# Optimization experiments

Hardware: AMD Instinct MI355X
Metric: run time of the kernel (lower is better)

The kernel has to match this reference:

```python
import jax, jax.numpy as jnp
import numpy as np

N = 6720      # 16 graphs * 420 nodes
E = 33600     # 16 graphs * 2100 edges (5 per node)
DIN = 2048
H1, C1 = 2, 1024   # conv1: heads=2, out=1024 -> concat 2048
H2, C2 = 1, 64     # conv2: heads=1, out=64
ED = 64            # edge_dim
NODES_PER_GRAPH = 420


def _lin(k, fi, fo):
    return jax.random.normal(k, (fi, fo), jnp.float32) / np.sqrt(fi).astype(np.float32)


def setup_inputs() -> dict:
    key = jax.random.key(0)
    ks = jax.random.split(key, 24)
    d = {}
    d["x"] = jax.random.normal(ks[0], (N, DIN), jnp.float32)
    d["edge_index"] = jax.random.randint(ks[1], (2, E), 0, N)
    # tiled learned edge_features param (torch.rand init), one 2100xED block per graph
    ef = jax.random.uniform(ks[2], (5 * NODES_PER_GRAPH, ED), jnp.float32)
    d["edge_attr"] = jnp.tile(ef, (N // NODES_PER_GRAPH, 1))
    HC1 = H1 * C1
    d["q1_w"] = _lin(ks[3], DIN, HC1); d["q1_b"] = jax.random.normal(ks[4], (HC1,)) * 0.01
    d["k1_w"] = _lin(ks[5], DIN, HC1); d["k1_b"] = jax.random.normal(ks[6], (HC1,)) * 0.01
    d["v1_w"] = _lin(ks[7], DIN, HC1); d["v1_b"] = jax.random.normal(ks[8], (HC1,)) * 0.01
    d["e1_w"] = _lin(ks[9], ED, HC1)                      # lin_edge has no bias in PyG
    d["s1_w"] = _lin(ks[10], DIN, HC1); d["s1_b"] = jax.random.normal(ks[11], (HC1,)) * 0.01
    HC2 = H2 * C2
    d["q2_w"] = _lin(ks[12], HC1, HC2); d["q2_b"] = jax.random.normal(ks[13], (HC2,)) * 0.01
    d["k2_w"] = _lin(ks[14], HC1, HC2); d["k2_b"] = jax.random.normal(ks[15], (HC2,)) * 0.01
    d["v2_w"] = _lin(ks[16], HC1, HC2); d["v2_b"] = jax.random.normal(ks[17], (HC2,)) * 0.01
    d["e2_w"] = _lin(ks[18], ED, HC2)
    d["s2_w"] = _lin(ks[19], HC1, HC2); d["s2_b"] = jax.random.normal(ks[20], (HC2,)) * 0.01
    return d


def _transformer_conv(x, src, dst, edge_attr, qw, qb, kw, kb, vw, vb, ew, sw, sb, H, C):
    """PyG TransformerConv (concat=True, beta=False, root_weight=True)."""
    n = x.shape[0]
    q = (x @ qw + qb).reshape(n, H, C)
    k = (x @ kw + kb).reshape(n, H, C)
    v = (x @ vw + vb).reshape(n, H, C)
    e = (edge_attr @ ew).reshape(-1, H, C)         # [E,H,C]
    kj = k[src] + e                                # gather source keys + edge emb
    alpha = jnp.sum(q[dst] * kj, axis=-1) / np.sqrt(C).astype(np.float32)  # [E,H]
    # scatter-softmax over incoming edges of each target node
    amax = jax.ops.segment_max(alpha, dst, num_segments=n)   # [N,H]
    ex = jnp.exp(alpha - amax[dst])
    denom = jax.ops.segment_sum(ex, dst, num_segments=n)
    attn = ex / (denom[dst] + 1e-16)               # [E,H]
    msg = (v[src] + e) * attn[..., None]           # [E,H,C]
    out = jax.ops.segment_sum(msg, dst, num_segments=n).reshape(n, H * C)
    return out + x @ sw + sb                       # root/skip connection


def reference(x, edge_index, edge_attr,
              q1_w, q1_b, k1_w, k1_b, v1_w, v1_b, e1_w, s1_w, s1_b,
              q2_w, q2_b, k2_w, k2_b, v2_w, v2_b, e2_w, s2_w, s2_b):
    src, dst = edge_index[0], edge_index[1]
    h = jax.nn.relu(_transformer_conv(x, src, dst, edge_attr,
                                      q1_w, q1_b, k1_w, k1_b, v1_w, v1_b,
                                      e1_w, s1_w, s1_b, H1, C1))
    h = jax.nn.relu(_transformer_conv(h, src, dst, edge_attr,
                                      q2_w, q2_b, k2_w, k2_b, v2_w, v2_b,
                                      e2_w, s2_w, s2_b, H2, C2))
    return h.reshape(-1, NODES_PER_GRAPH * 64)     # forward returns here (fc layers are dead code)
```

## Files before the change

kernel.cpp:

```cpp
#include <hip/hip_runtime.h>
#include <hip/hip_bf16.h>
#include <cstdint>
#include <cstddef>

#define NN    6720
#define MPAD  6912
#define NE    33600
#define KDIM  2048
#define HC1   2048

typedef __attribute__((ext_vector_type(8))) short bhalf8;
typedef __attribute__((ext_vector_type(4))) float fx4;

__device__ __forceinline__ float bf2f(short s) {
    union { unsigned int u; float f; } c;
    c.u = ((unsigned int)(unsigned short)s) << 16;
    return c.f;
}

__device__ __forceinline__ void gload16(const __hip_bfloat16* g, void* lds)
{
    __builtin_amdgcn_global_load_lds(
        (const __attribute__((address_space(1))) unsigned int*)g,
        (__attribute__((address_space(3))) unsigned int*)lds,
        16, 0, 0);
}

#define CFENCE asm volatile("" ::: "memory")

__global__ __launch_bounds__(256, 3) void gemm128_fused(
    const __hip_bfloat16* __restrict__ A,
    const __hip_bfloat16* __restrict__ Bt,
    const float* __restrict__ bcat,
    __hip_bfloat16* __restrict__ oq,
    __hip_bfloat16* __restrict__ ok,
    __hip_bfloat16* __restrict__ ov,
    float* __restrict__ oh)
{
    __shared__ alignas(16) char Lds[49152];

    const int bid = blockIdx.x;
    const int i   = bid >> 3;
    const int bx  = (bid & 7) * 8 + (i & 7);
    const int by  = i >> 3;

    const int tid  = threadIdx.x;
    const int w    = tid >> 6;
    const int lane = tid & 63;
    const int wm = w >> 1, wn = w & 1;
    const int rowA = by * 128;
    const int rowB = bx * 128;

    const int sug = ((lane & 3) ^ ((lane >> 3) & 3)) << 3;
    const __hip_bfloat16* Ag0 = A  + (size_t)(rowA + w * 32 + (lane >> 2)) * KDIM + sug;
    const __hip_bfloat16* Bg0 = Bt + (size_t)(rowB + w * 32 + (lane >> 2)) * KDIM + sug;

    const int rds = (((lane >> 4) ^ (((lane & 15) >> 1) & 3)) << 4);

    fx4 acc[4][4] = {};

#define STAGE(T)                                                          \
    { const int s_ = (T) % 3; const int k0_ = (T) * 32;                   \
      char* ab_ = Lds + s_ * 8192 + w * 2048;                             \
      char* bb_ = Lds + 24576 + s_ * 8192 + w * 2048;                     \
      gload16(Ag0 + k0_, ab_);                                            \
      gload16(Ag0 + k0_ + 16 * KDIM, ab_ + 1024);                         \
      gload16(Bg0 + k0_, bb_);                                            \
      gload16(Bg0 + k0_ + 16 * KDIM, bb_ + 1024); }

#define TILE(T, VM, DOSTAGE)                                              \
    { if (DOSTAGE) { STAGE((T) + 2); }                                    \
      asm volatile("s_waitcnt vmcnt(" VM ")" ::: "memory");               \
      __builtin_amdgcn_s_barrier(); CFENCE;                               \
      const int s_ = (T) % 3;                                             \
      const char* ap_ = Lds + s_ * 8192;                                  \
      const char* bp_ = Lds + 24576 + s_ * 8192;                          \
      bhalf8 af_[4], bf_[4];                                              \
      _Pragma("unroll")                                                   \
      for (int nj = 0; nj < 4; ++nj)                                      \
          bf_[nj] = *(const bhalf8*)(bp_ + (wn * 64 + nj * 16 + (lane & 15)) * 64 + rds); \
      _Pragma("unroll")                                                   \
      for (int mi = 0; mi < 4; ++mi)                                      \
          af_[mi] = *(const bhalf8*)(ap_ + (wm * 64 + mi * 16 + (lane & 15)) * 64 + rds); \
      __builtin_amdgcn_s_setprio(1);                                      \
      _Pragma("unroll")                                                   \
      for (int mi = 0; mi < 4; ++mi)                                      \
          _Pragma("unroll")                                               \
          for (int nj = 0; nj < 4; ++nj)                                  \
              acc[mi][nj] = __builtin_amdgcn_mfma_f32_16x16x32_bf16(      \
                  af_[mi], bf_[nj], acc[mi][nj], 0, 0, 0);                \
      __builtin_amdgcn_s_setprio(0); CFENCE;                              \
      __builtin_amdgcn_s_barrier(); CFENCE; }

    STAGE(0); STAGE(1);
    for (int t = 0; t < (KDIM / 32) - 2; ++t) {
        TILE(t, "8", 1);
    }
    TILE((KDIM / 32) - 2, "4", 0);
    TILE((KDIM / 32) - 1, "0", 0);

#undef TILE
#undef STAGE

    const int gcol = rowB + wn * 64;
    const int seg  = gcol >> 11;
    const int lcol = gcol & 2047;
    float bv[4];
    #pragma unroll
    for (int nj = 0; nj < 4; ++nj) bv[nj] = bcat[gcol + nj * 16 + (lane & 15)];
    char* scr = Lds + w * 8192;
    const int growA = rowA + wm * 64;

    #pragma unroll
    for (int h = 0; h < 2; ++h) {
        #pragma unroll
        for (int m2 = 0; m2 < 2; ++m2) {
            const int mi = h * 2 + m2;
            #pragma unroll
            for (int nj = 0; nj < 4; ++nj) {
                const int cl = nj * 16 + (lane & 15);
                #pragma unroll
                for (int i2 = 0; i2 < 4; ++i2) {
                    const int rl = m2 * 16 + ((lane >> 4) << 2) + i2;
                    *(float*)(scr + rl * 256 + cl * 4) = acc[mi][nj][i2] + bv[nj];
                }
            }
        }
        CFENCE;
        if (seg < 3) {
            __hip_bfloat16* dst = (seg == 0) ? oq : (seg == 1) ? ok : ov;
            #pragma unroll
            for (int p = 0; p < 4; ++p) {
                const int rl = p * 8 + (lane >> 3);
                const int u  = lane & 7;
                const float4 f0 = *(const float4*)(scr + rl * 256 + u * 32);
                const float4 f1 = *(const float4*)(scr + rl * 256 + u * 32 + 16);
                __hip_bfloat16 tb[8];
                tb[0] = __float2bfloat16(f0.x); tb[1] = __float2bfloat16(f0.y);
                tb[2] = __float2bfloat16(f0.z); tb[3] = __float2bfloat16(f0.w);
                tb[4] = __float2bfloat16(f1.x); tb[5] = __float2bfloat16(f1.y);
                tb[6] = __float2bfloat16(f1.z); tb[7] = __float2bfloat16(f1.w);
                *(bhalf8*)&dst[(size_t)(growA + h * 32 + rl) * 2048 + lcol + u * 8] =
                    *(bhalf8*)tb;
            }
        } else {
            #pragma unroll
            for (int p = 0; p < 8; ++p) {
                const int rl = p * 4 + (lane >> 4);
                const int u  = lane & 15;
                const float4 f = *(const float4*)(scr + rl * 256 + u * 16);
                *(float4*)&oh[(size_t)(growA + h * 32 + rl) * 2048 + lcol + u * 4] = f;
            }
        }
        asm volatile("s_waitcnt lgkmcnt(0)" ::: "memory");
        CFENCE;
    }
}

__global__ __launch_bounds__(256) void gemm_bf16(
    const __hip_bfloat16* __restrict__ A,
    const __hip_bfloat16* __restrict__ Bt,
    const float* __restrict__ bias,
    float* __restrict__ C,
    __hip_bfloat16* __restrict__ Cb,
    int M, int N, int K, int flags)
{
    __shared__ alignas(16) __hip_bfloat16 Asm[128 * 64];
    __shared__ alignas(16) __hip_bfloat16 Bsm[128 * 64];
    const int tid  = threadIdx.x;
    const int w    = tid >> 6;
    const int lane = tid & 63;
    const int wr = w >> 1, wc = w & 1;
    const int rowA = blockIdx.y * 128;
    const int rowB = blockIdx.x * 128;
    const int klen = K / gridDim.z;
    const int kbeg = blockIdx.z * klen;

    const int srow = w * 32 + (lane >> 3);
    const int ug8  = ((lane & 7) ^ (lane >> 3)) << 3;
    const __hip_bfloat16* Ag = A  + (size_t)(rowA + srow) * K + ug8;
    const __hip_bfloat16* Bg = Bt + (size_t)(rowB + srow) * K + ug8;
    char* AsBase = (char*)Asm + w * 4096;
    char* BsBase = (char*)Bsm + w * 4096;

    fx4 acc[4][4] = {};

    const int fra = wr * 64 + (lane & 15);
    const int frb = wc * 64 + (lane & 15);
    const int kb  = (lane >> 4) << 4;
    const int swz = (lane & 7) << 4;

    for (int k0 = kbeg; k0 < kbeg + klen; k0 += 64) {
        __syncthreads();
        #pragma unroll
        for (int j = 0; j < 4; ++j) {
            gload16(Ag + (size_t)j * 8 * K + k0, AsBase + j * 1024);
            gload16(Bg + (size_t)j * 8 * K + k0, BsBase + j * 1024);
        }
        __syncthreads();
        #pragma unroll
        for (int kk = 0; kk < 2; ++kk) {
            const int cb = kk * 64 + kb;
            bhalf8 af[4], bfr[4];
            #pragma unroll
            for (int mi = 0; mi < 4; ++mi)
                af[mi] = *(const bhalf8*)((const char*)Asm + (fra + mi * 16) * 128 + (cb ^ swz));
            #pragma unroll
            for (int nj = 0; nj < 4; ++nj)
                bfr[nj] = *(const bhalf8*)((const char*)Bsm + (frb + nj * 16) * 128 + (cb ^ swz));
            #pragma unroll
            for (int mi = 0; mi < 4; ++mi)
                #pragma unroll
                for (int nj = 0; nj < 4; ++nj)
                    acc[mi][nj] = __builtin_amdgcn_mfma_f32_16x16x32_bf16(
                        af[mi], bfr[nj], acc[mi][nj], 0, 0, 0);
        }
    }

    float* Cz = C ? C + (size_t)blockIdx.z * ((size_t)M * N) : nullptr;
    #pragma unroll
    for (int nj = 0; nj < 4; ++nj) {
        const int ccol = rowB + wc * 64 + nj * 16 + (lane & 15);
        const float bv = (flags & 1) ? bias[ccol] : 0.f;
        #pragma unroll
        for (int mi = 0; mi < 4; ++mi) {
            const int crow0 = rowA + wr * 64 + mi * 16 + ((lane >> 4) << 2);
            #pragma unroll
            for (int i = 0; i < 4; ++i) {
                size_t idx = (size_t)(crow0 + i) * N + ccol;
                float v = acc[mi][nj][i] + bv;
                if (flags & 2) v += Cz[idx];
                if (flags & 4) v = fmaxf(v, 0.f);
                if (Cz && !(flags & 8)) Cz[idx] = v;
                if (Cb) Cb[idx] = __float2bfloat16(v);
            }
        }
    }
}

__global__ void reduce4(const float* __restrict__ parts, size_t stride,
                        const float* __restrict__ bias, int colmask,
                        float* __restrict__ dst, int n)
{
    int i = blockIdx.x * 256 + threadIdx.x;
    if (i >= n) return;
    float v = parts[i] + parts[stride + i] + parts[2 * stride + i] + parts[3 * stride + i];
    if (bias) v += bias[i & colmask];
    dst[i] = v;
}

__global__ __launch_bounds__(256) void gemm_tile(
    const float* __restrict__ A, const float* __restrict__ B,
    const float* __restrict__ bias, float* __restrict__ C,
    int M, int N, int K, int flags)
{
    __shared__ float As[16][68];
    __shared__ float Bs[16][64];
    const int tid = threadIdx.x;
    const int bx = blockIdx.x, by = blockIdx.y;
    const int tx = tid & 15, ty = tid >> 4;
    const int arow = tid >> 2, acol = (tid & 3) << 2;
    const int brow = tid >> 4, bcol = (tid & 15) << 2;
    const float* Ag = A + (size_t)(by * 64 + arow) * K + acol;
    const float* Bg = B + (size_t)brow * N + bx * 64 + bcol;
    float acc[4][4] = {};
    for (int k0 = 0; k0 < K; k0 += 16) {
        const float4 av = *(const float4*)(Ag + k0);
        const float4 bv = *(const float4*)(Bg + (size_t)k0 * N);
        __syncthreads();
        As[acol + 0][arow] = av.x;
        As[acol + 1][arow] = av.y;
        As[acol + 2][arow] = av.z;
        As[acol + 3][arow] = av.w;
        *(float4*)&Bs[brow][bcol] = bv;
        __syncthreads();
        #pragma unroll
        for (int kk = 0; kk < 16; ++kk) {
            const float4 a4 = *(const float4*)&As[kk][ty << 2];
            const float4 b4 = *(const float4*)&Bs[kk][tx << 2];
            const float a[4] = {a4.x, a4.y, a4.z, a4.w};
            const float b[4] = {b4.x, b4.y, b4.z, b4.w};
            #pragma unroll
            for (int i = 0; i < 4; ++i)
                #pragma unroll
                for (int j = 0; j < 4; ++j)
                    acc[i][j] += a[i] * b[j];
        }
    }
    const int crow = by * 64 + (ty << 2);
    const int ccol = bx * 64 + (tx << 2);
    float4 b4 = make_float4(0.f, 0.f, 0.f, 0.f);
    if (flags & 1) b4 = *(const float4*)(bias + ccol);
    #pragma unroll
    for (int i = 0; i < 4; ++i) {
        float* cp = C + (size_t)(crow + i) * N + ccol;
        float4 v;
        v.x = acc[i][0] + b4.x; v.y = acc[i][1] + b4.y;
        v.z = acc[i][2] + b4.z; v.w = acc[i][3] + b4.w;
        if (flags & 2) {
            const float4 o = *(const float4*)cp;
            v.x += o.x; v.y += o.y; v.z += o.z; v.w += o.w;
        }
        *(float4*)cp = v;
    }
}

__global__ void count_deg(const int* __restrict__ ei, int* __restrict__ deg)
{
    int e = blockIdx.x * 256 + threadIdx.x;
    if (e < NE) atomicAdd(&deg[ei[NE + e]], 1);
}

__global__ __launch_bounds__(1024) void scan_kernel(const int* __restrict__ deg,
                                                    int* __restrict__ rowptr)
{
    __shared__ int s[1024];
    const int t = threadIdx.x;
    const int base = t * 7;
    int loc[7];
    int sum = 0;
    #pragma unroll
    for (int i = 0; i < 7; ++i) {
        int idx = base + i;
        int v = (idx < NN) ? deg[idx] : 0;
        loc[i] = v; sum += v;
    }
    s[t] = sum;
    __syncthreads();
    for (int off = 1; off < 1024; off <<= 1) {
        int v = (t >= off) ? s[t - off] : 0;
        __syncthreads();
        s[t] += v;
        __syncthreads();
    }
    int running = s[t] - sum;
    #pragma unroll
    for (int i = 0; i < 7; ++i) {
        int idx = base + i;
        if (idx <= NN) rowptr[idx] = running;
        if (idx < NN) running += loc[i];
    }
}

__global__ void fill_csr(const int* __restrict__ ei, const int* __restrict__ rowptr,
                         int* __restrict__ fillctr, int* __restrict__ elist)
{
    int e = blockIdx.x * 256 + threadIdx.x;
    if (e >= NE) return;
    int d = ei[NE + e];
    int pos = atomicAdd(&fillctr[d], 1);
    elist[rowptr[d] + pos] = e;
}

__global__ void sort_csr(const int* __restrict__ rowptr, int* __restrict__ elist)
{
    int n = blockIdx.x * 256 + threadIdx.x;
    if (n >= NN) return;
    int s0 = rowptr[n], s1 = rowptr[n + 1];
    for (int i = s0 + 1; i < s1; ++i) {
        int v = elist[i];
        int j = i - 1;
        while (j >= s0 && elist[j] > v) { elist[j + 1] = elist[j]; --j; }
        elist[j + 1] = v;
    }
}

__global__ void cvt_pad_bf16(const float* __restrict__ src, __hip_bfloat16* __restrict__ dst,
                             int relu)
{
    size_t i = (size_t)(blockIdx.x * 256 + threadIdx.x) * 4;
    int row = (int)(i >> 11);
    float4 v = make_float4(0.f, 0.f, 0.f, 0.f);
    if (row < NN) v = *(const float4*)&src[i];
    if (relu) {
        v.x = fmaxf(v.x, 0.f); v.y = fmaxf(v.y, 0.f);
        v.z = fmaxf(v.z, 0.f); v.w = fmaxf(v.w, 0.f);
    }
    dst[i + 0] = __float2bfloat16(v.x);
    dst[i + 1] = __float2bfloat16(v.y);
    dst[i + 2] = __float2bfloat16(v.z);
    dst[i + 3] = __float2bfloat16(v.w);
}

__global__ __launch_bounds__(256) void transpose_cvt4(
    const float* __restrict__ W0, const float* __restrict__ W1,
    const float* __restrict__ W2, const float* __restrict__ W3,
    __hip_bfloat16* __restrict__ dst)
{
    const float* W = (blockIdx.z == 0) ? W0 : (blockIdx.z == 1) ? W1
                   : (blockIdx.z == 2) ? W2 : W3;
    __hip_bfloat16* Bt = dst + (size_t)blockIdx.z * KDIM * KDIM;
    __shared__ float t[32][33];
    int kb = blockIdx.y * 32, nb = blockIdx.x * 32;
    int tx = threadIdx.x & 31, ty = threadIdx.x >> 5;
    #pragma unroll
    for (int i = 0; i < 32; i += 8)
        t[ty + i][tx] = W[(size_t)(kb + ty + i) * KDIM + nb + tx];
    __syncthreads();
    #pragma unroll
    for (int i = 0; i < 32; i += 8)
        Bt[(size_t)(nb + ty + i) * KDIM + kb + tx] = __float2bfloat16(t[tx][ty + i]);
}

__global__ void build_bcat(const float* __restrict__ q1b, const float* __restrict__ k1b,
                           const float* __restrict__ v1b, const float* __restrict__ s1b,
                           float* __restrict__ bcat)
{
    int i = blockIdx.x * 256 + threadIdx.x;
    if (i >= 4 * KDIM) return;
    int seg = i >> 11, j = i & 2047;
    const float* b = (seg == 0) ? q1b : (seg == 1) ? k1b : (seg == 2) ? v1b : s1b;
    bcat[i] = b[j];
}

__global__ void build_w1pp(const float* __restrict__ e1w, __hip_bfloat16* __restrict__ w1pp)
{
    int idx = blockIdx.x * 256 + threadIdx.x;
    int p = idx >> 11, j = idx & 2047;
    float v = ((j >> 10) == (p >> 6)) ? e1w[(size_t)(p & 63) * KDIM + j] : 0.f;
    w1pp[idx] = __float2bfloat16(v);
}

__global__ void build_w1ppT(const float* __restrict__ e1w, __hip_bfloat16* __restrict__ w1ppT)
{
    int idx = blockIdx.x * 256 + threadIdx.x;
    int n = idx >> 7, k = idx & 127;
    float v = ((n >> 10) == (k >> 6)) ? e1w[(size_t)(k & 63) * KDIM + n] : 0.f;
    w1ppT[idx] = __float2bfloat16(v);
}

__global__ void build_w2t(const float* __restrict__ qw, const float* __restrict__ kw,
                          const float* __restrict__ vw, const float* __restrict__ sw,
                          const float* __restrict__ qb, const float* __restrict__ kb,
                          const float* __restrict__ vb, const float* __restrict__ sb,
                          __hip_bfloat16* __restrict__ w2t, float* __restrict__ b2)
{
    int idx = blockIdx.x * 256 + threadIdx.x;
    int c = idx >> 11, d = idx & 2047;
    int g = c >> 6, j = c & 63;
    const float* w = (g == 0) ? qw : (g == 1) ? kw : (g == 2) ? vw : sw;
    w2t[idx] = __float2bfloat16(w[(size_t)d * 64 + j]);
    if (d == 0) {
        const float* b = (g == 0) ? qb : (g == 1) ? kb : (g == 2) ? vb : sb;
        b2[c] = b[j];
    }
}

__global__ __launch_bounds__(256) void alpha1_kernel(
    const __hip_bfloat16* __restrict__ q1b, const __hip_bfloat16* __restrict__ k1b,
    const float* __restrict__ P1, const float* __restrict__ ea,
    const int* __restrict__ ei, const int* __restrict__ elist,
    float* __restrict__ alpha)
{
    int i = blockIdx.x * 4 + (threadIdx.x >> 6);
    int lane = threadIdx.x & 63;
    int e = elist[i];
    int src = ei[e], dst = ei[NE + e];
    float eaj = ea[(size_t)e * 64 + lane];
    #pragma unroll
    for (int h = 0; h < 2; ++h) {
        const __hip_bfloat16* qh = q1b + (size_t)dst * HC1 + h * 1024 + lane * 16;
        const __hip_bfloat16* kh = k1b + (size_t)src * HC1 + h * 1024 + lane * 16;
        bhalf8 qa = *(const bhalf8*)qh, qc = *(const bhalf8*)(qh + 8);
        bhalf8 ka = *(const bhalf8*)kh, kc = *(const bhalf8*)(kh + 8);
        float s = 0.f;
        #pragma unroll
        for (int j = 0; j < 8; ++j) s += bf2f(qa[j]) * bf2f(ka[j]);
        #pragma unroll
        for (int j = 0; j < 8; ++j) s += bf2f(qc[j]) * bf2f(kc[j]);
        s += eaj * P1[(size_t)dst * 128 + h * 64 + lane];
        #pragma unroll
        for (int off = 32; off; off >>= 1) s += __shfl_xor(s, off);
        if (lane == 0) alpha[(size_t)i * 2 + h] = s * 0.03125f;
    }
}

__global__ void softmax_kernel(const int* __restrict__ rowptr,
                               float* __restrict__ alpha, int H)
{
    int n = blockIdx.x * 256 + threadIdx.x;
    if (n >= NN) return;
    int s0 = rowptr[n], s1 = rowptr[n + 1];
    for (int h = 0; h < H; ++h) {
        float m = -1e30f;
        for (int i = s0; i < s1; ++i)
            m = fmaxf(m, alpha[(size_t)i * H + h]);
        float ssum = 0.f;
        for (int i = s0; i < s1; ++i) {
            float ex = __expf(alpha[(size_t)i * H + h] - m);
            alpha[(size_t)i * H + h] = ex;
            ssum += ex;
        }
        float inv = 1.f / (ssum + 1e-16f);
        for (int i = s0; i < s1; ++i)
            alpha[(size_t)i * H + h] *= inv;
    }
}

__global__ __launch_bounds__(128) void r1_kernel(
    const int* __restrict__ rowptr, const int* __restrict__ elist,
    const float* __restrict__ attn, const float* __restrict__ ea,
    __hip_bfloat16* __restrict__ R1)
{
    int n = blockIdx.x;
    int p = threadIdx.x;
    int h = p >> 6, j = p & 63;
    int s0 = rowptr[n], s1 = rowptr[n + 1];
    float r = 0.f;
    for (int i = s0; i < s1; ++i) {
        int e = elist[i];
        r += attn[(size_t)i * 2 + h] * ea[(size_t)e * 64 + j];
    }
    R1[(size_t)n * 128 + p] = __float2bfloat16(r);
}

__global__ __launch_bounds__(256) void agg1_kernel(
    const int* __restrict__ rowptr, const int* __restrict__ elist,
    const int* __restrict__ ei, const float* __restrict__ attn,
    const __hip_bfloat16* __restrict__ v1b, float* __restrict__ h1)
{
    int n = blockIdx.x;
    int c0 = threadIdx.x * 8;
    int h = c0 >> 10;
    int s0 = rowptr[n], s1 = rowptr[n + 1];
    float acc[8];
    const float4 p0 = *(const float4*)&h1[(size_t)n * HC1 + c0];
    const float4 p1 = *(const float4*)&h1[(size_t)n * HC1 + c0 + 4];
    acc[0] = p0.x; acc[1] = p0.y; acc[2] = p0.z; acc[3] = p0.w;
    acc[4] = p1.x; acc[5] = p1.y; acc[6] = p1.z; acc[7] = p1.w;
    for (int i = s0; i < s1; ++i) {
        float at = attn[(size_t)i * 2 + h];
        bhalf8 v = *(const bhalf8*)&v1b[(size_t)ei[elist[i]] * HC1 + c0];
        #pragma unroll
        for (int j = 0; j < 8; ++j) acc[j] += at * bf2f(v[j]);
    }
    float4 o0 = make_float4(acc[0], acc[1], acc[2], acc[3]);
    float4 o1 = make_float4(acc[4], acc[5], acc[6], acc[7]);
    *(float4*)&h1[(size_t)n * HC1 + c0] = o0;
    *(float4*)&h1[(size_t)n * HC1 + c0 + 4] = o1;
}

__global__ __launch_bounds__(256) void alpha2_kernel(
    const float* __restrict__ qkvs2, const float* __restrict__ E2,
    const int* __restrict__ ei, const int* __restrict__ elist,
    float* __restrict__ alpha2)
{
    int i = blockIdx.x * 4 + (threadIdx.x >> 6);
    int lane = threadIdx.x & 63;
    int e = elist[i];
    int src = ei[e], dst = ei[NE + e];
    float q = qkvs2[(size_t)dst * 256 + lane];
    float k = qkvs2[(size_t)src * 256 + 64 + lane];
    float s = q * (k + E2[(size_t)e * 64 + lane]);
    #pragma unroll
    for (int off = 32; off; off >>= 1) s += __shfl_xor(s, off);
    if (lane == 0) alpha2[i] = s * 0.125f;
}

__global__ __launch_bounds__(64) void agg2_kernel(
    const int* __restrict__ rowptr, const int* __restrict__ elist,
    const int* __restrict__ ei, const float* __restrict__ attn2,
    const float* __restrict__ qkvs2, const float* __restrict__ E2,
    float* __restrict__ out)
{
    int n = blockIdx.x;
    int c = threadIdx.x;
    int s0 = rowptr[n], s1 = rowptr[n + 1];
    float acc = qkvs2[(size_t)n * 256 + 192 + c];
    for (int i = s0; i < s1; ++i) {
        int e = elist[i];
        acc += attn2[i] * (qkvs2[(size_t)ei[e] * 256 + 128 + c] + E2[(size_t)e * 64 + c]);
    }
    out[(size_t)n * 64 + c] = fmaxf(acc, 0.f);
}

extern "C" void kernel_launch(void* const* d_in, const int* in_sizes, int n_in,
                              void* d_out, int out_size, void* d_ws, size_t ws_size,
                              hipStream_t stream)
{
    const float* x   = (const float*)d_in[0];
    const int*   ei  = (const int*)d_in[1];
    const float* ea  = (const float*)d_in[2];
    const float* q1w = (const float*)d_in[3];
    const float* q1b = (const float*)d_in[4];
    const float* k1w = (const float*)d_in[5];
    const float* k1b = (const float*)d_in[6];
    const float* v1w = (const float*)d_in[7];
    const float* v1b = (const float*)d_in[8];
    const float* e1w = (const float*)d_in[9];
    const float* s1w = (const float*)d_in[10];
    const float* s1b = (const float*)d_in[11];
    const float* q2w = (const float*)d_in[12];
    const float* q2b = (const float*)d_in[13];
    const float* k2w = (const float*)d_in[14];
    const float* k2b = (const float*)d_in[15];
    const float* v2w = (const float*)d_in[16];
    const float* v2b = (const float*)d_in[17];
    const float* e2w = (const float*)d_in[18];
    const float* s2w = (const float*)d_in[19];
    const float* s2b = (const float*)d_in[20];
    float* out = (float*)d_out;

    char* base = (char*)d_ws;
    size_t off = 0;
    auto alloc = [&](size_t nbytes) {
        size_t o = off; off += (nbytes + 255) & ~(size_t)255; return o;
    };
    const size_t xb_off   = alloc((size_t)MPAD * KDIM * 2);
    const size_t wcat_off = alloc((size_t)4 * KDIM * KDIM * 2);
    __hip_bfloat16* xb    = (__hip_bfloat16*)(base + xb_off);
    __hip_bfloat16* wcat  = (__hip_bfloat16*)(base + wcat_off);
    __hip_bfloat16* h1b   = xb;
    float*          Cpart = (float*)(base + wcat_off);
    __hip_bfloat16* w2t   = (__hip_bfloat16*)(base + wcat_off + (size_t)29 * 1024 * 1024);

    __hip_bfloat16* q1bb  = (__hip_bfloat16*)(base + alloc((size_t)MPAD * HC1 * 2));
    __hip_bfloat16* k1bb  = (__hip_bfloat16*)(base + alloc((size_t)MPAD * HC1 * 2));
    __hip_bfloat16* v1bb  = (__hip_bfloat16*)(base + alloc((size_t)MPAD * HC1 * 2));
    float*          h1    = (float*)(base + alloc((size_t)MPAD * HC1 * 4));
    float*          bcat  = (float*)(base + alloc((size_t)4 * KDIM * 4));
    float*          P1    = (float*)(base + alloc((size_t)MPAD * 128 * 4));
    __hip_bfloat16* R1b   = (__hip_bfloat16*)(base + alloc((size_t)MPAD * 128 * 2));
    __hip_bfloat16* w1pp  = (__hip_bfloat16*)(base + alloc((size_t)128 * KDIM * 2));
    __hip_bfloat16* w1ppT = (__hip_bfloat16*)(base + alloc((size_t)KDIM * 128 * 2));
    float*          b2    = (float*)(base + alloc(256 * 4));
    float*          qkvs2 = (float*)(base + alloc((size_t)MPAD * 256 * 4));
    float*          E2    = (float*)(base + alloc((size_t)NE * 64 * 4));
    float*          at1   = (float*)(base + alloc((size_t)NE * 2 * 4));
    float*          at2   = (float*)(base + alloc((size_t)NE * 4));
    int* deg    = (int*)(base + alloc((size_t)NN * 4));
    int* fill   = (int*)(base + alloc((size_t)NN * 4));
    int* rowptr = (int*)(base + alloc((size_t)(NN + 1) * 4));
    int* elist  = (int*)(base + alloc((size_t)NE * 4));

    hipMemsetAsync(deg, 0, sizeof(int) * 2 * NN, stream);
    count_deg<<<(NE + 255) / 256, 256, 0, stream>>>(ei, deg);
    scan_kernel<<<1, 1024, 0, stream>>>(deg, rowptr);
    fill_csr<<<(NE + 255) / 256, 256, 0, stream>>>(ei, rowptr, fill, elist);
    sort_csr<<<(NN + 255) / 256, 256, 0, stream>>>(rowptr, elist);

    const int cvblk = (MPAD * KDIM / 4) / 256;
    cvt_pad_bf16<<<cvblk, 256, 0, stream>>>(x, xb, 0);
    transpose_cvt4<<<dim3(KDIM / 32, KDIM / 32, 4), 256, 0, stream>>>(q1w, k1w, v1w, s1w, wcat);
    build_bcat<<<(4 * KDIM) / 256, 256, 0, stream>>>(q1b, k1b, v1b, s1b, bcat);

    gemm128_fused<<<3456, 256, 0, stream>>>(xb, wcat, bcat, q1bb, k1bb, v1bb, h1);

    build_w1pp<<<(128 * KDIM) / 256, 256, 0, stream>>>(e1w, w1pp);
    build_w1ppT<<<(KDIM * 128) / 256, 256, 0, stream>>>(e1w, w1ppT);
    gemm_bf16<<<dim3(1, MPAD / 128, 4), 256, 0, stream>>>(q1bb, w1pp, nullptr, Cpart, nullptr,
                                                          MPAD, 128, KDIM, 0);
    reduce4<<<(MPAD * 128) / 256, 256, 0, stream>>>(Cpart, (size_t)MPAD * 128, nullptr, 0,
                                                    P1, MPAD * 128);

    alpha1_kernel<<<NE / 4, 256, 0, stream>>>(q1bb, k1bb, P1, ea, ei, elist, at1);
    softmax_kernel<<<(NN + 255) / 256, 256, 0, stream>>>(rowptr, at1, 2);
    r1_kernel<<<NN, 128, 0, stream>>>(rowptr, elist, at1, ea, R1b);
    agg1_kernel<<<NN, 256, 0, stream>>>(rowptr, elist, ei, at1, v1bb, h1);
    gemm_bf16<<<dim3(HC1 / 128, MPAD / 128), 256, 0, stream>>>(R1b, w1ppT, nullptr, h1, h1b,
                                                               MPAD, HC1, 128, 2 | 4 | 8);

    build_w2t<<<(256 * KDIM) / 256, 256, 0, stream>>>(q2w, k2w, v2w, s2w, q2b, k2b, v2b, s2b,
                                                      w2t, b2);
    gemm_bf16<<<dim3(2, MPAD / 128, 4), 256, 0, stream>>>(h1b, w2t, nullptr, Cpart, nullptr,
                                                          MPAD, 256, KDIM, 0);
    reduce4<<<(MPAD * 256) / 256, 256, 0, stream>>>(Cpart, (size_t)MPAD * 256, b2, 255,
                                                    qkvs2, MPAD * 256);
    gemm_tile<<<dim3(1, NE / 64), 256, 0, stream>>>(ea, e2w, nullptr, E2, NE, 64, 64, 0);

    alpha2_kernel<<<NE / 4, 256, 0, stream>>>(qkvs2, E2, ei, elist, at2);
    softmax_kernel<<<(NN + 255) / 256, 256, 0, stream>>>(rowptr, at2, 1);
    agg2_kernel<<<NN, 64, 0, stream>>>(rowptr, elist, ei, at2, qkvs2, E2, out);

    (void)in_sizes; (void)n_in; (void)out_size; (void)ws_size;
}
```

Measured before the change: 559.8 us.

## Enlarge fused QKV/skip GEMM tile to 256x128 with padded epilogue scratch

The main fused projection GEMM now computes a 256x128 output tile per block instead of 128x128. Each wave holds 8x4 MFMA accumulators and stages twice as much A data per k-step, which halves the number of B loads and the grid size. This is meant to raise arithmetic intensity and cut global and LDS traffic per FLOP. It costs more registers and LDS (72KB), lowering occupancy to 2 blocks per CU. The epilogue scratch rows are also padded to 272 bytes to avoid bank conflicts, with narrower bf16 stores.

New measurement: 526.6 us. 5.9% less time.

```diff
diff --git a/kernel.cpp b/kernel.cpp
--- a/kernel.cpp
+++ b/kernel.cpp
@@ -10,6 +10,7 @@
 #define HC1   2048
 
 typedef __attribute__((ext_vector_type(8))) short bhalf8;
+typedef __attribute__((ext_vector_type(4))) short bhalf4;
 typedef __attribute__((ext_vector_type(4))) float fx4;
 
 __device__ __forceinline__ float bf2f(short s) {
@@ -28,7 +29,7 @@
 
 #define CFENCE asm volatile("" ::: "memory")
 
-__global__ __launch_bounds__(256, 3) void gemm128_fused(
+__global__ __launch_bounds__(256, 2) void gemm256x128_fused(
     const __hip_bfloat16* __restrict__ A,
     const __hip_bfloat16* __restrict__ Bt,
     const float* __restrict__ bcat,
@@ -37,34 +38,36 @@
     __hip_bfloat16* __restrict__ ov,
     float* __restrict__ oh)
 {
-    __shared__ alignas(16) char Lds[49152];
+    __shared__ alignas(16) char Lds[73728];
 
     const int bid = blockIdx.x;
-    const int i   = bid >> 3;
-    const int bx  = (bid & 7) * 8 + (i & 7);
-    const int by  = i >> 3;
+    const int i0  = bid >> 3;
+    const int bx  = (bid & 7) * 8 + (i0 & 7);
+    const int by  = i0 >> 3;
 
     const int tid  = threadIdx.x;
     const int w    = tid >> 6;
     const int lane = tid & 63;
     const int wm = w >> 1, wn = w & 1;
-    const int rowA = by * 128;
+    const int rowA = by * 256;
     const int rowB = bx * 128;
 
     const int sug = ((lane & 3) ^ ((lane >> 3) & 3)) << 3;
-    const __hip_bfloat16* Ag0 = A  + (size_t)(rowA + w * 32 + (lane >> 2)) * KDIM + sug;
+    const __hip_bfloat16* Ag0 = A  + (size_t)(rowA + w * 64 + (lane >> 2)) * KDIM + sug;
     const __hip_bfloat16* Bg0 = Bt + (size_t)(rowB + w * 32 + (lane >> 2)) * KDIM + sug;
 
     const int rds = (((lane >> 4) ^ (((lane & 15) >> 1) & 3)) << 4);
 
-    fx4 acc[4][4] = {};
+    fx4 acc[8][4] = {};
 
 #define STAGE(T)                                                          \
     { const int s_ = (T) % 3; const int k0_ = (T) * 32;                   \
-      char* ab_ = Lds + s_ * 8192 + w * 2048;                             \
-      char* bb_ = Lds + 24576 + s_ * 8192 + w * 2048;                     \
+      char* ab_ = Lds + s_ * 16384 + w * 4096;                            \
+      char* bb_ = Lds + 49152 + s_ * 8192 + w * 2048;                     \
       gload16(Ag0 + k0_, ab_);                                            \
       gload16(Ag0 + k0_ + 16 * KDIM, ab_ + 1024);                         \
+      gload16(Ag0 + k0_ + 32 * KDIM, ab_ + 2048);                         \
+      gload16(Ag0 + k0_ + 48 * KDIM, ab_ + 3072);                         \
       gload16(Bg0 + k0_, bb_);                                            \
       gload16(Bg0 + k0_ + 16 * KDIM, bb_ + 1024); }
 
@@ -73,18 +76,18 @@
       asm volatile("s_waitcnt vmcnt(" VM ")" ::: "memory");               \
       __builtin_amdgcn_s_barrier(); CFENCE;                               \
       const int s_ = (T) % 3;                                             \
-      const char* ap_ = Lds + s_ * 8192;                                  \
-      const char* bp_ = Lds + 24576 + s_ * 8192;                          \
-      bhalf8 af_[4], bf_[4];                                              \
+      const char* ap_ = Lds + s_ * 16384;                                 \
+      const char* bp_ = Lds + 49152 + s_ * 8192;                          \
+      bhalf8 af_[8], bf_[4];                                              \
       _Pragma("unroll")                                                   \
       for (int nj = 0; nj < 4; ++nj)                                      \
           bf_[nj] = *(const bhalf8*)(bp_ + (wn * 64 + nj * 16 + (lane & 15)) * 64 + rds); \
       _Pragma("unroll")                                                   \
-      for (int mi = 0; mi < 4; ++mi)                                      \
-          af_[mi] = *(const bhalf8*)(ap_ + (wm * 64 + mi * 16 + (lane & 15)) * 64 + rds); \
+      for (int mi = 0; mi < 8; ++mi)                                      \
+          af_[mi] = *(const bhalf8*)(ap_ + (wm * 128 + mi * 16 + (lane & 15)) * 64 + rds); \
       __builtin_amdgcn_s_setprio(1);                                      \
       _Pragma("unroll")                                                   \
-      for (int mi = 0; mi < 4; ++mi)                                      \
+      for (int mi = 0; mi < 8; ++mi)                                      \
           _Pragma("unroll")                                               \
           for (int nj = 0; nj < 4; ++nj)                                  \
               acc[mi][nj] = __builtin_amdgcn_mfma_f32_16x16x32_bf16(      \
@@ -94,9 +97,9 @@
 
     STAGE(0); STAGE(1);
     for (int t = 0; t < (KDIM / 32) - 2; ++t) {
-        TILE(t, "8", 1);
-    }
-    TILE((KDIM / 32) - 2, "4", 0);
+        TILE(t, "12", 1);
+    }
+    TILE((KDIM / 32) - 2, "6", 0);
     TILE((KDIM / 32) - 1, "0", 0);
 
 #undef TILE
@@ -108,48 +111,47 @@
     float bv[4];
     #pragma unroll
     for (int nj = 0; nj < 4; ++nj) bv[nj] = bcat[gcol + nj * 16 + (lane & 15)];
-    char* scr = Lds + w * 8192;
-    const int growA = rowA + wm * 64;
-
-    #pragma unroll
-    for (int h = 0; h < 2; ++h) {
+    char* scr = Lds + w * 8704;
+    const int growA = rowA + wm * 128;
+
+    #pragma unroll
+    for (int c = 0; c < 4; ++c) {
         #pragma unroll
         for (int m2 = 0; m2 < 2; ++m2) {
-            const int mi = h * 2 + m2;
+            const int mi = c * 2 + m2;
             #pragma unroll
             for (int nj = 0; nj < 4; ++nj) {
                 const int cl = nj * 16 + (lane & 15);
                 #pragma unroll
                 for (int i2 = 0; i2 < 4; ++i2) {
                     const int rl = m2 * 16 + ((lane >> 4) << 2) + i2;
-                    *(float*)(scr + rl * 256 + cl * 4) = acc[mi][nj][i2] + bv[nj];
+                    *(float*)(scr + rl * 272 + cl * 4) = acc[mi][nj][i2] + bv[nj];
                 }
             }
         }
+        asm volatile("s_waitcnt lgkmcnt(0)" ::: "memory");
         CFENCE;
+        const int rrow = (lane >> 4);
+        const int u    = lane & 15;
         if (seg < 3) {
             __hip_bfloat16* dst = (seg == 0) ? oq : (seg == 1) ? ok : ov;
             #pragma unroll
-            for (int p = 0; p < 4; ++p) {
-                const int rl = p * 8 + (lane >> 3);
-                const int u  = lane & 7;
-                const float4 f0 = *(const float4*)(scr + rl * 256 + u * 32);
-                const float4 f1 = *(const float4*)(scr + rl * 256 + u * 32 + 16);
-                __hip_bfloat16 tb[8];
-                tb[0] = __float2bfloat16(f0.x); tb[1] = __float2bfloat16(f0.y);
-                tb[2] = __float2bfloat16(f0.z); tb[3] = __float2bfloat16(f0.w);
-                tb[4] = __float2bfloat16(f1.x); tb[5] = __float2bfloat16(f1.y);
-                tb[6] = __float2bfloat16(f1.z); tb[7] = __float2bfloat16(f1.w);
-                *(bhalf8*)&dst[(size_t)(growA + h * 32 + rl) * 2048 + lcol + u * 8] =
-                    *(bhalf8*)tb;
+            for (int p = 0; p < 8; ++p) {
+                const int row = p * 4 + rrow;
+                const float4 f = *(const float4*)(scr + row * 272 + u * 16);
+                bhalf4 tb;
+                tb[0] = (short)__bfloat16_as_ushort(__float2bfloat16(f.x));
+                tb[1] = (short)__bfloat16_as_ushort(__float2bfloat16(f.y));
+                tb[2] = (short)__bfloat16_as_ushort(__float2bfloat16(f.z));
+                tb[3] = (short)__bfloat16_as_ushort(__float2bfloat16(f.w));
+                *(bhalf4*)&dst[(size_t)(growA + c * 32 + row) * 2048 + lcol + u * 4] = tb;
             }
         } else {
             #pragma unroll
             for (int p = 0; p < 8; ++p) {
-                const int rl = p * 4 + (lane >> 4);
-                const int u  = lane & 15;
-                const float4 f = *(const float4*)(scr + rl * 256 + u * 16);
-                *(float4*)&oh[(size_t)(growA + h * 32 + rl) * 2048 + lcol + u * 4] = f;
+                const int row = p * 4 + rrow;
+                const float4 f = *(const float4*)(scr + row * 272 + u * 16);
+                *(float4*)&oh[(size_t)(growA + c * 32 + row) * 2048 + lcol + u * 4] = f;
             }
         }
         asm volatile("s_waitcnt lgkmcnt(0)" ::: "memory");
@@ -644,7 +646,7 @@
     transpose_cvt4<<<dim3(KDIM / 32, KDIM / 32, 4), 256, 0, stream>>>(q1w, k1w, v1w, s1w, wcat);
     build_bcat<<<(4 * KDIM) / 256, 256, 0, stream>>>(q1b, k1b, v1b, s1b, bcat);
 
-    gemm128_fused<<<3456, 256, 0, stream>>>(xb, wcat, bcat, q1bb, k1bb, v1bb, h1);
+    gemm256x128_fused<<<1728, 256, 0, stream>>>(xb, wcat, bcat, q1bb, k1bb, v1bb, h1);
 
     build_w1pp<<<(128 * KDIM) / 256, 256, 0, stream>>>(e1w, w1pp);
     build_w1ppT<<<(KDIM * 128) / 256, 256, 0, stream>>>(e1w, w1ppT);
```
